# Kernel tuning notes

Hardware: AMD Instinct MI355X
Metric: run time of the kernel (lower is better)

## Reference

```python
import jax, jax.numpy as jnp
import numpy as np

N_NODES = 50000
N_EDGES = 800000
D_IN = 128
D_OUT = 128


def setup_inputs() -> dict:
    key = jax.random.key(0)
    k1, k2, k3, k4, k5, k6 = jax.random.split(key, 6)
    x = jax.random.normal(k1, (N_NODES, D_IN), dtype=jnp.float32)
    weight = jax.random.normal(k2, (D_IN, D_OUT), dtype=jnp.float32)
    bias = jax.random.normal(k3, (D_OUT,), dtype=jnp.float32)
    adj_row = jax.random.randint(k4, (N_EDGES,), 0, N_NODES, dtype=jnp.int64)
    adj_col = jax.random.randint(k5, (N_EDGES,), 0, N_NODES, dtype=jnp.int64)
    adj_val = jax.random.uniform(k6, (N_EDGES,), dtype=jnp.float32)
    return {"x": x, "weight": weight, "bias": bias,
            "adj_row": adj_row, "adj_col": adj_col, "adj_val": adj_val}


def reference(x, weight, bias, adj_row, adj_col, adj_val):
    # support = x @ W  -- dense GEMM [N, D_in] x [D_in, D_out]
    support = jnp.matmul(x, weight)
    # spmm(adj, support): out[i] = sum_e adj_val[e] * support[adj_col[e]] for adj_row[e]==i
    messages = support[adj_col] * adj_val[:, None]          # [E, D_out]
    output = jax.ops.segment_sum(messages, adj_row, num_segments=x.shape[0])
    return output + bias
```

## Files before the change

### kernel.cpp

```cpp
#include <hip/hip_runtime.h>

#define D 128
#define ELL_CAP 64
#define EPT 8

typedef __attribute__((ext_vector_type(8))) short short8;
typedef __attribute__((ext_vector_type(4))) float floatx4;
typedef unsigned int uint;
typedef unsigned short ushort;

__device__ inline short f2bf(float f) {
  unsigned u = __float_as_uint(f);
  u += 0x7FFF + ((u >> 16) & 1);
  return (short)(u >> 16);
}

__global__ __launch_bounds__(256) void gemm_mfma_kernel(const float* __restrict__ x,
                                                        const float* __restrict__ w,
                                                        ushort* __restrict__ support,
                                                        int n_nodes) {
  __shared__ short sWA[4 * 8 * 64 * 8];
  const int tid = threadIdx.x;

  const float4* w4 = (const float4*)w;
  for (int t = tid; t < D * D / 4; t += 256) {
    float4 v = w4[t];
    int k = t >> 5;
    int m0 = (t & 31) * 4;
    int kt = k >> 5, quad = (k >> 3) & 3, j = k & 7;
    float vv[4] = {v.x, v.y, v.z, v.w};
#pragma unroll
    for (int u = 0; u < 4; ++u) {
      int m = m0 + u;
      int mt = m >> 4, nid = m & 15;
      sWA[((kt * 8 + mt) * 64 + quad * 16 + nid) * 8 + j] = f2bf(vv[u]);
    }
  }
  __syncthreads();

  const int wid = tid >> 6;
  const int lane = tid & 63;
  const int quad = lane >> 4;
  const int node = blockIdx.x * 64 + wid * 16 + (lane & 15);
  const bool ok = (node < n_nodes);

  floatx4 acc[8];
#pragma unroll
  for (int mt = 0; mt < 8; ++mt) acc[mt] = (floatx4){0.f, 0.f, 0.f, 0.f};

#pragma unroll
  for (int kt = 0; kt < 4; ++kt) {
    short8 b = (short8){0, 0, 0, 0, 0, 0, 0, 0};
    if (ok) {
      const float4 v0 = *(const float4*)&x[(size_t)node * D + kt * 32 + quad * 8];
      const float4 v1 = *(const float4*)&x[(size_t)node * D + kt * 32 + quad * 8 + 4];
      b = (short8){f2bf(v0.x), f2bf(v0.y), f2bf(v0.z), f2bf(v0.w),
                   f2bf(v1.x), f2bf(v1.y), f2bf(v1.z), f2bf(v1.w)};
    }
#pragma unroll
    for (int mt = 0; mt < 8; ++mt) {
      short8 a = *(const short8*)&sWA[((kt * 8 + mt) * 64 + lane) * 8];
      acc[mt] = __builtin_amdgcn_mfma_f32_16x16x32_bf16(a, b, acc[mt], 0, 0, 0);
    }
  }

  if (ok) {
#pragma unroll
    for (int mt = 0; mt < 8; ++mt) {
      uint lo = ((uint)(ushort)f2bf(acc[mt][1]) << 16) | (ushort)f2bf(acc[mt][0]);
      uint hi = ((uint)(ushort)f2bf(acc[mt][3]) << 16) | (ushort)f2bf(acc[mt][2]);
      *(uint2*)&support[(size_t)node * D + mt * 16 + quad * 4] = make_uint2(lo, hi);
    }
  }
}

__global__ __launch_bounds__(256) void ell_scatter_kernel(const int* __restrict__ adj_row,
                                                          const int* __restrict__ adj_col,
                                                          const float* __restrict__ adj_val,
                                                          int* __restrict__ cnt,
                                                          uint* __restrict__ ell,
                                                          int n_edges, int range_size) {
  const int g = blockIdx.x & 7;
  const int c = blockIdx.x >> 3;
  const int lo = g * range_size, hi = lo + range_size;
  const int base = c * (256 * EPT) + threadIdx.x * EPT;

  if (base + EPT <= n_edges) {
    int4 r0 = *(const int4*)&adj_row[base];
    int4 r1 = *(const int4*)&adj_row[base + 4];
    int4 c0 = *(const int4*)&adj_col[base];
    int4 c1 = *(const int4*)&adj_col[base + 4];
    float4 v0 = *(const float4*)&adj_val[base];
    float4 v1 = *(const float4*)&adj_val[base + 4];
    int rr[EPT] = {r0.x, r0.y, r0.z, r0.w, r1.x, r1.y, r1.z, r1.w};
    int cc[EPT] = {c0.x, c0.y, c0.z, c0.w, c1.x, c1.y, c1.z, c1.w};
    float vv[EPT] = {v0.x, v0.y, v0.z, v0.w, v1.x, v1.y, v1.z, v1.w};
#pragma unroll
    for (int u = 0; u < EPT; ++u) {
      int r = rr[u];
      if (r >= lo && r < hi) {
        int pos = atomicAdd(&cnt[r], 1);
        if (pos < ELL_CAP)
          ell[(size_t)r * ELL_CAP + pos] = ((uint)cc[u] << 16) | (ushort)f2bf(vv[u]);
      }
    }
  } else {
    for (int u = 0; u < EPT; ++u) {
      int e = base + u;
      if (e >= n_edges) break;
      int r = adj_row[e];
      if (r >= lo && r < hi) {
        int pos = atomicAdd(&cnt[r], 1);
        if (pos < ELL_CAP)
          ell[(size_t)r * ELL_CAP + pos] = ((uint)adj_col[e] << 16) | (ushort)f2bf(adj_val[e]);
      }
    }
  }
}

__global__ __launch_bounds__(256) void spmm_ell_kernel(const int* __restrict__ cnt,
                                                       const uint* __restrict__ ell,
                                                       const uint* __restrict__ sup,
                                                       const float* __restrict__ bias,
                                                       float* __restrict__ out,
                                                       int n_rows) {
  int wave = (int)((blockIdx.x * 256 + threadIdx.x) >> 6);
  int lane = threadIdx.x & 63;
  if (wave >= n_rows) return;
  const int r = wave;
  int n = cnt[r];
  if (n > ELL_CAP) n = ELL_CAP;
  uint ent = 0;
  if (lane < n) ent = ell[(size_t)r * ELL_CAP + lane];
  float ax = 0.f, ay = 0.f;
  int j = 0;
  for (; j + 4 <= n; j += 4) {
    uint e0 = __shfl(ent, j + 0);
    uint e1 = __shfl(ent, j + 1);
    uint e2 = __shfl(ent, j + 2);
    uint e3 = __shfl(ent, j + 3);
    uint s0 = sup[(size_t)(e0 >> 16) * 64 + lane];
    uint s1 = sup[(size_t)(e1 >> 16) * 64 + lane];
    uint s2 = sup[(size_t)(e2 >> 16) * 64 + lane];
    uint s3 = sup[(size_t)(e3 >> 16) * 64 + lane];
    float w0 = __uint_as_float(e0 << 16);
    float w1 = __uint_as_float(e1 << 16);
    float w2 = __uint_as_float(e2 << 16);
    float w3 = __uint_as_float(e3 << 16);
    ax = fmaf(w0, __uint_as_float(s0 << 16), ax);
    ay = fmaf(w0, __uint_as_float(s0 & 0xffff0000u), ay);
    ax = fmaf(w1, __uint_as_float(s1 << 16), ax);
    ay = fmaf(w1, __uint_as_float(s1 & 0xffff0000u), ay);
    ax = fmaf(w2, __uint_as_float(s2 << 16), ax);
    ay = fmaf(w2, __uint_as_float(s2 & 0xffff0000u), ay);
    ax = fmaf(w3, __uint_as_float(s3 << 16), ax);
    ay = fmaf(w3, __uint_as_float(s3 & 0xffff0000u), ay);
  }
  for (; j < n; ++j) {
    uint e0 = __shfl(ent, j);
    uint s0 = sup[(size_t)(e0 >> 16) * 64 + lane];
    float w0 = __uint_as_float(e0 << 16);
    ax = fmaf(w0, __uint_as_float(s0 << 16), ax);
    ay = fmaf(w0, __uint_as_float(s0 & 0xffff0000u), ay);
  }
  float2 b = *(const float2*)&bias[lane * 2];
  *(float2*)&out[(size_t)r * D + lane * 2] = make_float2(b.x + ax, b.y + ay);
}

extern "C" void kernel_launch(void* const* d_in, const int* in_sizes, int n_in,
                              void* d_out, int out_size, void* d_ws, size_t ws_size,
                              hipStream_t stream) {
  const float* x       = (const float*)d_in[0];
  const float* w       = (const float*)d_in[1];
  const float* bias    = (const float*)d_in[2];
  const int*   adj_row = (const int*)d_in[3];
  const int*   adj_col = (const int*)d_in[4];
  const float* adj_val = (const float*)d_in[5];

  const int n_nodes = in_sizes[0] / D;
  const int n_edges = in_sizes[3];
  float* out = (float*)d_out;

  char* ws = (char*)d_ws;
  ushort* support = (ushort*)ws; ws += ((size_t)n_nodes * D * 2 + 15) & ~15ull;
  int*    row_cnt = (int*)ws;    ws += ((size_t)n_nodes * 4 + 15) & ~15ull;
  uint*   ell     = (uint*)ws;   ws += (size_t)n_nodes * ELL_CAP * 4;

  hipMemsetAsync(row_cnt, 0, (size_t)n_nodes * 4, stream);

  int gemm_blocks = (n_nodes + 63) / 64;
  gemm_mfma_kernel<<<gemm_blocks, 256, 0, stream>>>(x, w, support, n_nodes);

  const int range_size = (n_nodes + 7) / 8;
  const int chunks = (n_edges + 256 * EPT - 1) / (256 * EPT);
  ell_scatter_kernel<<<chunks * 8, 256, 0, stream>>>(adj_row, adj_col, adj_val,
                                                     row_cnt, ell, n_edges, range_size);

  int spmm_blocks = (n_nodes + 3) / 4;
  spmm_ell_kernel<<<spmm_blocks, 256, 0, stream>>>(row_cnt, ell, (const uint*)support,
                                                   bias, out, n_nodes);
}
```

Baseline: 177.5 us.

## Fuse GEMM and ELL scatter into one launch; unroll SpMM gather by eight

The independent dense GEMM and the edge-to-ELL scatter now run as one kernel launch, split by block index, so their blocks can run on the GPU at the same time. This removes one launch and the idle gap between the two stages. The SpMM loop now rounds the row length up to a multiple of eight and issues eight support-row gathers before any FMA, to keep more loads in flight. Padded slots hold zero entries, so they read row 0 with zero weight, which costs a little extra traffic. The fused kernel reserves the GEMM's shared-memory footprint for every block, which may lower occupancy for the scatter blocks.

```diff
diff --git a/kernel.cpp b/kernel.cpp
--- a/kernel.cpp
+++ b/kernel.cpp
@@ -15,104 +15,102 @@
   return (short)(u >> 16);
 }
 
-__global__ __launch_bounds__(256) void gemm_mfma_kernel(const float* __restrict__ x,
-                                                        const float* __restrict__ w,
-                                                        ushort* __restrict__ support,
-                                                        int n_nodes) {
+__global__ __launch_bounds__(256) void gemm_scatter_kernel(
+    const float* __restrict__ x, const float* __restrict__ w,
+    ushort* __restrict__ support, int n_nodes, int gemm_blocks,
+    const int* __restrict__ adj_row, const int* __restrict__ adj_col,
+    const float* __restrict__ adj_val, int* __restrict__ cnt,
+    uint* __restrict__ ell, int n_edges, int range_size) {
   __shared__ short sWA[4 * 8 * 64 * 8];
   const int tid = threadIdx.x;
 
-  const float4* w4 = (const float4*)w;
-  for (int t = tid; t < D * D / 4; t += 256) {
-    float4 v = w4[t];
-    int k = t >> 5;
-    int m0 = (t & 31) * 4;
-    int kt = k >> 5, quad = (k >> 3) & 3, j = k & 7;
-    float vv[4] = {v.x, v.y, v.z, v.w};
+  if ((int)blockIdx.x < gemm_blocks) {
+    const float4* w4 = (const float4*)w;
+    for (int t = tid; t < D * D / 4; t += 256) {
+      float4 v = w4[t];
+      int k = t >> 5;
+      int m0 = (t & 31) * 4;
+      int kt = k >> 5, quad = (k >> 3) & 3, j = k & 7;
+      float vv[4] = {v.x, v.y, v.z, v.w};
 #pragma unroll
-    for (int u = 0; u < 4; ++u) {
-      int m = m0 + u;
-      int mt = m >> 4, nid = m & 15;
-      sWA[((kt * 8 + mt) * 64 + quad * 16 + nid) * 8 + j] = f2bf(vv[u]);
+      for (int u = 0; u < 4; ++u) {
+        int m = m0 + u;
+        int mt = m >> 4, nid = m & 15;
+        sWA[((kt * 8 + mt) * 64 + quad * 16 + nid) * 8 + j] = f2bf(vv[u]);
+      }
     }
-  }
-  __syncthreads();
+    __syncthreads();
 
-  const int wid = tid >> 6;
-  const int lane = tid & 63;
-  const int quad = lane >> 4;
-  const int node = blockIdx.x * 64 + wid * 16 + (lane & 15);
-  const bool ok = (node < n_nodes);
+    const int wid = tid >> 6;
+    const int lane = tid & 63;
+    const int quad = lane >> 4;
+    const int node = blockIdx.x * 64 + wid * 16 + (lane & 15);
+    const bool ok = (node < n_nodes);
 
-  floatx4 acc[8];
+    floatx4 acc[8];
 #pragma unroll
-  for (int mt = 0; mt < 8; ++mt) acc[mt] = (floatx4){0.f, 0.f, 0.f, 0.f};
+    for (int mt = 0; mt < 8; ++mt) acc[mt] = (floatx4){0.f, 0.f, 0.f, 0.f};
 
 #pragma unroll
-  for (int kt = 0; kt < 4; ++kt) {
-    short8 b = (short8){0, 0, 0, 0, 0, 0, 0, 0};
+    for (int kt = 0; kt < 4; ++kt) {
+      short8 b = (short8){0, 0, 0, 0, 0, 0, 0, 0};
+      if (ok) {
+        const float4 v0 = *(const float4*)&x[(size_t)node * D + kt * 32 + quad * 8];
+        const float4 v1 = *(const float4*)&x[(size_t)node * D + kt * 32 + quad * 8 + 4];
+        b = (short8){f2bf(v0.x), f2bf(v0.y), f2bf(v0.z), f2bf(v0.w),
+                     f2bf(v1.x), f2bf(v1.y), f2bf(v1.z), f2bf(v1.w)};
+      }
+#pragma unroll
+      for (int mt = 0; mt < 8; ++mt) {
+        short8 a = *(const short8*)&sWA[((kt * 8 + mt) * 64 + lane) * 8];
+        acc[mt] = __builtin_amdgcn_mfma_f32_16x16x32_bf16(a, b, acc[mt], 0, 0, 0);
+      }
+    }
+
     if (ok) {
-      const float4 v0 = *(const float4*)&x[(size_t)node * D + kt * 32 + quad * 8];
-      const float4 v1 = *(const float4*)&x[(size_t)node * D + kt * 32 + quad * 8 + 4];
-      b = (short8){f2bf(v0.x), f2bf(v0.y), f2bf(v0.z), f2bf(v0.w),
-                   f2bf(v1.x), f2bf(v1.y), f2bf(v1.z), f2bf(v1.w)};
-    }
 #pragma unroll
-    for (int mt = 0; mt < 8; ++mt) {
-      short8 a = *(const short8*)&sWA[((kt * 8 + mt) * 64 + lane) * 8];
-      acc[mt] = __builtin_amdgcn_mfma_f32_16x16x32_bf16(a, b, acc[mt], 0, 0, 0);
-    }
-  }
-
-  if (ok) {
-#pragma unroll
-    for (int mt = 0; mt < 8; ++mt) {
-      uint lo = ((uint)(ushort)f2bf(acc[mt][1]) << 16) | (ushort)f2bf(acc[mt][0]);
-      uint hi = ((uint)(ushort)f2bf(acc[mt][3]) << 16) | (ushort)f2bf(acc[mt][2]);
-      *(uint2*)&support[(size_t)node * D + mt * 16 + quad * 4] = make_uint2(lo, hi);
-    }
-  }
-}
-
-__global__ __launch_bounds__(256) void ell_scatter_kernel(const int* __restrict__ adj_row,
-                                                          const int* __restrict__ adj_col,
-                                                          const float* __restrict__ adj_val,
-                                                          int* __restrict__ cnt,
-                                                          uint* __restrict__ ell,
-                                                          int n_edges, int range_size) {
-  const int g = blockIdx.x & 7;
-  const int c = blockIdx.x >> 3;
-  const int lo = g * range_size, hi = lo + range_size;
-  const int base = c * (256 * EPT) + threadIdx.x * EPT;
-
-  if (base + EPT <= n_edges) {
-    int4 r0 = *(const int4*)&adj_row[base];
-    int4 r1 = *(const int4*)&adj_row[base + 4];
-    int4 c0 = *(const int4*)&adj_col[base];
-    int4 c1 = *(const int4*)&adj_col[base + 4];
-    float4 v0 = *(const float4*)&adj_val[base];
-    float4 v1 = *(const float4*)&adj_val[base + 4];
-    int rr[EPT] = {r0.x, r0.y, r0.z, r0.w, r1.x, r1.y, r1.z, r1.w};
-    int cc[EPT] = {c0.x, c0.y, c0.z, c0.w, c1.x, c1.y, c1.z, c1.w};
-    float vv[EPT] = {v0.x, v0.y, v0.z, v0.w, v1.x, v1.y, v1.z, v1.w};
-#pragma unroll
-    for (int u = 0; u < EPT; ++u) {
-      int r = rr[u];
-      if (r >= lo && r < hi) {
-        int pos = atomicAdd(&cnt[r], 1);
-        if (pos < ELL_CAP)
-          ell[(size_t)r * ELL_CAP + pos] = ((uint)cc[u] << 16) | (ushort)f2bf(vv[u]);
+      for (int mt = 0; mt < 8; ++mt) {
+        uint lo = ((uint)(ushort)f2bf(acc[mt][1]) << 16) | (ushort)f2bf(acc[mt][0]);
+        uint hi = ((uint)(ushort)f2bf(acc[mt][3]) << 16) | (ushort)f2bf(acc[mt][2]);
+        *(uint2*)&support[(size_t)node * D + mt * 16 + quad * 4] = make_uint2(lo, hi);
       }
     }
   } else {
-    for (int u = 0; u < EPT; ++u) {
-      int e = base + u;
-      if (e >= n_edges) break;
-      int r = adj_row[e];
-      if (r >= lo && r < hi) {
-        int pos = atomicAdd(&cnt[r], 1);
-        if (pos < ELL_CAP)
-          ell[(size_t)r * ELL_CAP + pos] = ((uint)adj_col[e] << 16) | (ushort)f2bf(adj_val[e]);
+    const int b = blockIdx.x - gemm_blocks;
+    const int g = b & 7;
+    const int c = b >> 3;
+    const int lo = g * range_size, hi = lo + range_size;
+    const int base = c * (256 * EPT) + tid * EPT;
+
+    if (base + EPT <= n_edges) {
+      int4 r0 = *(const int4*)&adj_row[base];
+      int4 r1 = *(const int4*)&adj_row[base + 4];
+      int4 c0 = *(const int4*)&adj_col[base];
+      int4 c1 = *(const int4*)&adj_col[base + 4];
+      float4 v0 = *(const float4*)&adj_val[base];
+      float4 v1 = *(const float4*)&adj_val[base + 4];
+      int rr[EPT] = {r0.x, r0.y, r0.z, r0.w, r1.x, r1.y, r1.z, r1.w};
+      int cc[EPT] = {c0.x, c0.y, c0.z, c0.w, c1.x, c1.y, c1.z, c1.w};
+      float vv[EPT] = {v0.x, v0.y, v0.z, v0.w, v1.x, v1.y, v1.z, v1.w};
+#pragma unroll
+      for (int u = 0; u < EPT; ++u) {
+        int r = rr[u];
+        if (r >= lo && r < hi) {
+          int pos = atomicAdd(&cnt[r], 1);
+          if (pos < ELL_CAP)
+            ell[(size_t)r * ELL_CAP + pos] = ((uint)cc[u] << 16) | (ushort)f2bf(vv[u]);
+        }
+      }
+    } else {
+      for (int u = 0; u < EPT; ++u) {
+        int e = base + u;
+        if (e >= n_edges) break;
+        int r = adj_row[e];
+        if (r >= lo && r < hi) {
+          int pos = atomicAdd(&cnt[r], 1);
+          if (pos < ELL_CAP)
+            ell[(size_t)r * ELL_CAP + pos] = ((uint)adj_col[e] << 16) | (ushort)f2bf(adj_val[e]);
+        }
       }
     }
   }
@@ -133,35 +131,20 @@
   uint ent = 0;
   if (lane < n) ent = ell[(size_t)r * ELL_CAP + lane];
   float ax = 0.f, ay = 0.f;
-  int j = 0;
-  for (; j + 4 <= n; j += 4) {
-    uint e0 = __shfl(ent, j + 0);
-    uint e1 = __shfl(ent, j + 1);
-    uint e2 = __shfl(ent, j + 2);
-    uint e3 = __shfl(ent, j + 3);
-    uint s0 = sup[(size_t)(e0 >> 16) * 64 + lane];
-    uint s1 = sup[(size_t)(e1 >> 16) * 64 + lane];
-    uint s2 = sup[(size_t)(e2 >> 16) * 64 + lane];
-    uint s3 = sup[(size_t)(e3 >> 16) * 64 + lane];
-    float w0 = __uint_as_float(e0 << 16);
-    float w1 = __uint_as_float(e1 << 16);
-    float w2 = __uint_as_float(e2 << 16);
-    float w3 = __uint_as_float(e3 << 16);
-    ax = fmaf(w0, __uint_as_float(s0 << 16), ax);
-    ay = fmaf(w0, __uint_as_float(s0 & 0xffff0000u), ay);
-    ax = fmaf(w1, __uint_as_float(s1 << 16), ax);
-    ay = fmaf(w1, __uint_as_float(s1 & 0xffff0000u), ay);
-    ax = fmaf(w2, __uint_as_float(s2 << 16), ax);
-    ay = fmaf(w2, __uint_as_float(s2 & 0xffff0000u), ay);
-    ax = fmaf(w3, __uint_as_float(s3 << 16), ax);
-    ay = fmaf(w3, __uint_as_float(s3 & 0xffff0000u), ay);
-  }
-  for (; j < n; ++j) {
-    uint e0 = __shfl(ent, j);
-    uint s0 = sup[(size_t)(e0 >> 16) * 64 + lane];
-    float w0 = __uint_as_float(e0 << 16);
-    ax = fmaf(w0, __uint_as_float(s0 << 16), ax);
-    ay = fmaf(w0, __uint_as_float(s0 & 0xffff0000u), ay);
+  const int m = (n + 7) & ~7;
+  for (int j = 0; j < m; j += 8) {
+    uint e[8];
+    uint s[8];
+#pragma unroll
+    for (int u = 0; u < 8; ++u) e[u] = __shfl(ent, j + u);
+#pragma unroll
+    for (int u = 0; u < 8; ++u) s[u] = sup[(size_t)(e[u] >> 16) * 64 + lane];
+#pragma unroll
+    for (int u = 0; u < 8; ++u) {
+      float wv = __uint_as_float(e[u] << 16);
+      ax = fmaf(wv, __uint_as_float(s[u] << 16), ax);
+      ay = fmaf(wv, __uint_as_float(s[u] & 0xffff0000u), ay);
+    }
   }
   float2 b = *(const float2*)&bias[lane * 2];
   *(float2*)&out[(size_t)r * D + lane * 2] = make_float2(b.x + ax, b.y + ay);
@@ -188,13 +171,12 @@
 
   hipMemsetAsync(row_cnt, 0, (size_t)n_nodes * 4, stream);
 
-  int gemm_blocks = (n_nodes + 63) / 64;
-  gemm_mfma_kernel<<<gemm_blocks, 256, 0, stream>>>(x, w, support, n_nodes);
-
+  const int gemm_blocks = (n_nodes + 63) / 64;
   const int range_size = (n_nodes + 7) / 8;
   const int chunks = (n_edges + 256 * EPT - 1) / (256 * EPT);
-  ell_scatter_kernel<<<chunks * 8, 256, 0, stream>>>(adj_row, adj_col, adj_val,
-                                                     row_cnt, ell, n_edges, range_size);
+  gemm_scatter_kernel<<<gemm_blocks + chunks * 8, 256, 0, stream>>>(
+      x, w, support, n_nodes, gemm_blocks,
+      adj_row, adj_col, adj_val, row_cnt, ell, n_edges, range_size);
 
   int spmm_blocks = (n_nodes + 3) / 4;
   spmm_ell_kernel<<<spmm_blocks, 256, 0, stream>>>(row_cnt, ell, (const uint*)support,
```

Measured after the change: 157.3 us. -11.4%, faster.
